# Optimization experiments

Hardware: AMD Instinct MI355X
Metric: run time of the kernel (lower is better)

## Reference

```python
import jax, jax.numpy as jnp
import numpy as np

B, M, D, H, C = 256, 512, 768, 8, 768


def setup_inputs() -> dict:
    key = jax.random.key(0)
    ks = jax.random.split(key, 12)
    rn = lambda k, shp, s=1.0: jax.random.normal(k, shp, dtype=jnp.float32) * s
    w = 1.0 / np.sqrt(D)
    return dict(
        controller_state=rn(ks[0], (B, C)),
        write_data=rn(ks[1], (B, D)),
        memory=rn(ks[2], (M, D), 0.1),
        in_proj_w=rn(ks[3], (3 * D, D), w), in_proj_b=jnp.zeros((3 * D,), jnp.float32),
        out_w=rn(ks[4], (D, D), w), out_b=jnp.zeros((D,), jnp.float32),
        read_w=rn(ks[5], (D, C), w), read_b=jnp.zeros((D,), jnp.float32),
        write_w=rn(ks[6], (D, C), w), write_b=jnp.zeros((D,), jnp.float32),
        erase_w=rn(ks[7], (D, C), w), erase_b=jnp.zeros((D,), jnp.float32),
        ug_w=rn(ks[8], (1, C + D), w), ug_b=jnp.zeros((1,), jnp.float32),
        fg_w=rn(ks[9], (1, C + D), w), fg_b=jnp.zeros((1,), jnp.float32),
    )


def _mha(q, kv, in_proj_w, in_proj_b, out_w, out_b, num_heads):
    # q: [B,1,D] query, kv: [B,M,D] keys=values. Matches torch.nn.MultiheadAttention
    # (batch_first, eval mode -> no dropout, average_attn_weights=True).
    b, m, d = kv.shape
    dh = d // num_heads
    wq, wk, wv = jnp.split(in_proj_w, 3, axis=0)
    bq, bk, bv = jnp.split(in_proj_b, 3, axis=0)
    qh = (q @ wq.T + bq).reshape(b, 1, num_heads, dh).transpose(0, 2, 1, 3)   # [B,H,1,dh]
    kh = (kv @ wk.T + bk).reshape(b, m, num_heads, dh).transpose(0, 2, 1, 3)  # [B,H,M,dh]
    vh = (kv @ wv.T + bv).reshape(b, m, num_heads, dh).transpose(0, 2, 1, 3)
    scores = jnp.einsum('bhqd,bhkd->bhqk', qh, kh) / jnp.sqrt(jnp.float32(dh))
    attn = jax.nn.softmax(scores, axis=-1)                                    # [B,H,1,M]
    ctx = jnp.einsum('bhqk,bhkd->bhqd', attn, vh)
    ctx = ctx.transpose(0, 2, 1, 3).reshape(b, 1, d)
    out = ctx @ out_w.T + out_b
    return out, attn.mean(axis=1)  # out [B,1,D], weights averaged over heads [B,1,M]


def reference(controller_state, write_data, memory, in_proj_w, in_proj_b,
              out_w, out_b, read_w, read_b, write_w, write_b,
              erase_w, erase_b, ug_w, ug_b, fg_w, fg_b):
    b = controller_state.shape[0]
    memory_batch = jnp.broadcast_to(memory[None], (b,) + memory.shape)        # [B,M,D]

    read_key = (controller_state @ read_w.T + read_b)[:, None, :]             # [B,1,D]
    read_data, _ = _mha(read_key, memory_batch, in_proj_w, in_proj_b, out_w, out_b, H)
    read_data = read_data[:, 0, :]                                            # [B,D]

    write_key = (controller_state @ write_w.T + write_b)[:, None, :]
    erase_vec = jax.nn.sigmoid(controller_state @ erase_w.T + erase_b)[:, None, :]  # [B,1,D]
    _, write_weights = _mha(write_key, memory_batch, in_proj_w, in_proj_b, out_w, out_b, H)
    ww = write_weights[:, 0, :]                                               # [B,M]

    combined = jnp.concatenate([controller_state, read_data], axis=-1)        # [B,C+D]
    ug = jax.nn.sigmoid(combined @ ug_w.T + ug_b)                             # [B,1]
    fg = jax.nn.sigmoid(combined @ fg_w.T + fg_b)                             # [B,1]

    erase_term = ww[:, :, None] * erase_vec * fg[:, :, None]                  # [B,M,D]
    write_term = ww[:, :, None] * write_data[:, None, :] * ug[:, :, None]     # [B,M,D]
    updated_memory = memory_batch + (write_term - erase_term)
    return read_data, updated_memory
```

## Files before the change

### kernel.cpp

```cpp
#include <hip/hip_runtime.h>
#include <math.h>

#define B_ 256
#define M_ 512
#define D_ 768
#define H_ 8
#define DH_ 96
#define C_ 768

typedef float  f32x4_t __attribute__((ext_vector_type(4)));
typedef short  s16x8   __attribute__((ext_vector_type(8)));
typedef unsigned short u16;

__device__ __forceinline__ u16 cvt_bf16(float f) {
    union { float f; unsigned int u; } v; v.f = f;
    unsigned int r = (v.u + 0x7FFFu + ((v.u >> 16) & 1u)) >> 16;
    return (u16)r;
}
__device__ __forceinline__ float bf16_f32(u16 h) {
    union { unsigned int u; float f; } v; v.u = ((unsigned int)h) << 16;
    return v.f;
}

#define ACC_INIT {{0,0,0,0},{0,0,0,0},{0,0,0,0},{0,0,0,0}}

__global__ __launch_bounds__(256) void conv_bf16(
    const float* __restrict__ mem, const float* __restrict__ cs,
    const float* __restrict__ ipw, const float* __restrict__ rw,
    const float* __restrict__ www, const float* __restrict__ ew,
    const float* __restrict__ outw,
    u16* __restrict__ memb, u16* __restrict__ csb, u16* __restrict__ ipwb,
    u16* __restrict__ rwb, u16* __restrict__ wwwb, u16* __restrict__ ewb,
    u16* __restrict__ outwb)
{
    const int bid = blockIdx.x;
    const float* src; u16* dst; int base;
    if      (bid < 192)  { src = mem;  dst = memb;  base = bid; }
    else if (bid < 288)  { src = cs;   dst = csb;   base = bid - 192; }
    else if (bid < 1152) { src = ipw;  dst = ipwb;  base = bid - 288; }
    else if (bid < 1440) { src = rw;   dst = rwb;   base = bid - 1152; }
    else if (bid < 1728) { src = www;  dst = wwwb;  base = bid - 1440; }
    else if (bid < 2016) { src = ew;   dst = ewb;   base = bid - 1728; }
    else                 { src = outw; dst = outwb; base = bid - 2016; }
    const size_t i = ((size_t)base * 256 + threadIdx.x) * 8;
    float4 x = *reinterpret_cast<const float4*>(src + i);
    float4 y = *reinterpret_cast<const float4*>(src + i + 4);
    s16x8 o;
    o[0]=cvt_bf16(x.x); o[1]=cvt_bf16(x.y); o[2]=cvt_bf16(x.z); o[3]=cvt_bf16(x.w);
    o[4]=cvt_bf16(y.x); o[5]=cvt_bf16(y.y); o[6]=cvt_bf16(y.z); o[7]=cvt_bf16(y.w);
    *reinterpret_cast<s16x8*>(dst + i) = o;
}

template<int BK>
__device__ __forceinline__ void mm64b(
    const u16* __restrict__ A, int lda, const u16* __restrict__ B, int ldb,
    int ksteps, int bRowClamp, u16* lA, u16* lB, f32x4_t* acc, int nfrag)
{
    constexpr int NL = BK / 32;
    const int t = threadIdx.x;
    const int srow = t >> 2, kq = t & 3;
    const int l = t & 63, w = t >> 6;
    const int brow = srow < bRowClamp ? srow : bRowClamp;

    for (int ks = 0; ks < ksteps; ++ks) {
        s16x8 va[NL], vb[NL];
        #pragma unroll
        for (int c = 0; c < NL; ++c) {
            const int ko = ks * BK + (kq * NL + c) * 8;
            va[c] = *reinterpret_cast<const s16x8*>(A + (size_t)srow * lda + ko);
            vb[c] = *reinterpret_cast<const s16x8*>(B + (size_t)brow * ldb + ko);
        }
        __syncthreads();
        #pragma unroll
        for (int c = 0; c < NL; ++c) {
            const int kb = kq * NL + c;
            *reinterpret_cast<s16x8*>(lA + (kb * 64 + srow) * 8) = va[c];
            *reinterpret_cast<s16x8*>(lB + (kb * 64 + srow) * 8) = vb[c];
        }
        __syncthreads();
        #pragma unroll
        for (int ksub = 0; ksub < NL; ++ksub) {
            const int kb = (l >> 4) + ksub * 4;
            s16x8 af = *reinterpret_cast<const s16x8*>(lA + (kb * 64 + w * 16 + (l & 15)) * 8);
            #pragma unroll
            for (int nb = 0; nb < 4; ++nb) {
                if (nb < nfrag) {
                    s16x8 bf = *reinterpret_cast<const s16x8*>(lB + (kb * 64 + nb * 16 + (l & 15)) * 8);
                    acc[nb] = __builtin_amdgcn_mfma_f32_16x16x32_bf16(af, bf, acc[nb], 0, 0, 0);
                }
            }
        }
    }
}

__device__ __forceinline__ void epilogue_f32(
    const f32x4_t* acc, float* out, int ldo, int m0, int n0,
    const float* bias, int act, int nfrag)
{
    const int t = threadIdx.x, l = t & 63, w = t >> 6;
    const int mbase = m0 + w * 16 + (l >> 4) * 4;
    #pragma unroll
    for (int nb = 0; nb < 4; ++nb) {
        if (nb >= nfrag) break;
        const int col = n0 + nb * 16 + (l & 15);
        const float bv = bias ? bias[col] : 0.0f;
        #pragma unroll
        for (int r = 0; r < 4; ++r) {
            float v = acc[nb][r] + bv;
            if (act) v = 1.0f / (1.0f + expf(-v));
            out[(size_t)(mbase + r) * ldo + col] = v;
        }
    }
}

__device__ __forceinline__ void epilogue_bf16(
    const f32x4_t* acc, u16* out, int ldo, int m0, int n0,
    const float* bias, float scale, int nfrag)
{
    const int t = threadIdx.x, l = t & 63, w = t >> 6;
    const int mbase = m0 + w * 16 + (l >> 4) * 4;
    #pragma unroll
    for (int nb = 0; nb < 4; ++nb) {
        if (nb >= nfrag) break;
        const int col = n0 + nb * 16 + (l & 15);
        const float bv = bias ? bias[col] : 0.0f;
        #pragma unroll
        for (int r = 0; r < 4; ++r)
            out[(size_t)(mbase + r) * ldo + col] = cvt_bf16(acc[nb][r] * scale + bv);
    }
}

__global__ __launch_bounds__(256) void stage1_mfma(
    const u16* __restrict__ memb, const u16* __restrict__ csb,
    const u16* __restrict__ ipwb, const float* __restrict__ ipb,
    const u16* __restrict__ rwb, const float* __restrict__ rb,
    const u16* __restrict__ wwwb, const float* __restrict__ ww_b,
    const u16* __restrict__ ewb, const float* __restrict__ eb,
    u16* __restrict__ khb, u16* __restrict__ vhT,
    u16* __restrict__ rwkeysb, float* __restrict__ erase)
{
    __shared__ u16 lA[8192], lB[8192];
    f32x4_t acc[4] = ACC_INIT;
    const int bid = blockIdx.x;
    if (bid < 192) {
        const int mt = bid / 24, nt = bid % 24;
        mm64b<64>(memb + (size_t)mt * 64 * 768, 768,
                  ipwb + (size_t)768 * 768 + (size_t)nt * 64 * 768, 768,
                  12, 63, lA, lB, acc, 4);
        const int t = threadIdx.x, l = t & 63, w = t >> 6;
        const int mbase = mt * 64 + w * 16 + (l >> 4) * 4;
        if (nt < 12) {
            #pragma unroll
            for (int nb = 0; nb < 4; ++nb) {
                const int col = nt * 64 + nb * 16 + (l & 15);
                const float bv = ipb[768 + col];
                #pragma unroll
                for (int r = 0; r < 4; ++r)
                    khb[(size_t)(mbase + r) * 768 + col] = cvt_bf16(acc[nb][r] + bv);
            }
        } else {
            #pragma unroll
            for (int nb = 0; nb < 4; ++nb) {
                const int cg = (nt - 12) * 64 + nb * 16 + (l & 15);
                const int h = cg / 96, d = cg % 96;
                const float bv = ipb[1536 + cg];
                u16* dst = vhT + ((size_t)h * 96 + d) * 512;
                #pragma unroll
                for (int r = 0; r < 4; ++r)
                    dst[mbase + r] = cvt_bf16(acc[nb][r] + bv);
            }
        }
    } else if (bid < 240) {
        const int lid = bid - 192, mt = lid / 12, nt = lid % 12;
        mm64b<64>(csb + (size_t)mt * 64 * 768, 768, rwb + (size_t)nt * 64 * 768, 768,
                  12, 63, lA, lB, acc, 4);
        epilogue_bf16(acc, rwkeysb, 768, mt * 64, nt * 64, rb, 1.0f, 4);
    } else if (bid < 288) {
        const int lid = bid - 240, mt = lid / 12, nt = lid % 12;
        mm64b<64>(csb + (size_t)mt * 64 * 768, 768, wwwb + (size_t)nt * 64 * 768, 768,
                  12, 63, lA, lB, acc, 4);
        epilogue_bf16(acc, rwkeysb + (size_t)256 * 768, 768, mt * 64, nt * 64, ww_b, 1.0f, 4);
    } else {
        const int lid = bid - 288, mt = lid / 12, nt = lid % 12;
        mm64b<64>(csb + (size_t)mt * 64 * 768, 768, ewb + (size_t)nt * 64 * 768, 768,
                  12, 63, lA, lB, acc, 4);
        epilogue_f32(acc, erase, 768, mt * 64, nt * 64, eb, 1, 4);
    }
}

__global__ __launch_bounds__(256) void stage2_mfma(
    const u16* __restrict__ rwkeysb, const u16* __restrict__ ipwb,
    const float* __restrict__ ipb, u16* __restrict__ qrwb)
{
    __shared__ u16 lA[8192], lB[8192];
    f32x4_t acc[4] = ACC_INIT;
    const int mt = blockIdx.x / 12, nt = blockIdx.x % 12;
    mm64b<64>(rwkeysb + (size_t)mt * 64 * 768, 768, ipwb + (size_t)nt * 64 * 768, 768,
              12, 63, lA, lB, acc, 4);
    epilogue_bf16(acc, qrwb, 768, mt * 64, nt * 64, ipb, 1.0f, 4);
}

__global__ __launch_bounds__(256) void scores_mfma(
    const u16* __restrict__ qrwb, const u16* __restrict__ khb, u16* __restrict__ S)
{
    __shared__ u16 lA[4096], lB[4096];
    f32x4_t acc[4] = ACC_INIT;
    const int h = blockIdx.y;
    const int mt = blockIdx.x >> 3, nt = blockIdx.x & 7;
    mm64b<32>(qrwb + (size_t)mt * 64 * 768 + h * 96, 768,
              khb + (size_t)nt * 64 * 768 + h * 96, 768, 3, 63, lA, lB, acc, 4);
    epilogue_bf16(acc, S + (size_t)h * 512 * 512, 512, mt * 64, nt * 64,
                  nullptr, 0.10206207261596577f, 4);
}

__global__ __launch_bounds__(256) void softmax_rows(
    const u16* __restrict__ S, u16* __restrict__ Pr, float* __restrict__ attnw)
{
    const int rid = blockIdx.x, h = rid >> 9, q = rid & 511, t = threadIdx.x;
    __shared__ float red4[4];
    const u16* s = S + (size_t)rid * 512;
    const float s0 = bf16_f32(s[t]), s1 = bf16_f32(s[t + 256]);
    float v = fmaxf(s0, s1);
    #pragma unroll
    for (int off = 32; off > 0; off >>= 1) v = fmaxf(v, __shfl_xor(v, off));
    if ((t & 63) == 0) red4[t >> 6] = v;
    __syncthreads();
    const float mx = fmaxf(fmaxf(red4[0], red4[1]), fmaxf(red4[2], red4[3]));
    float e0 = expf(s0 - mx), e1 = expf(s1 - mx);
    float sum = e0 + e1;
    #pragma unroll
    for (int off = 32; off > 0; off >>= 1) sum += __shfl_xor(sum, off);
    __syncthreads();
    if ((t & 63) == 0) red4[t >> 6] = sum;
    __syncthreads();
    const float inv = 1.0f / (red4[0] + red4[1] + red4[2] + red4[3]);
    e0 *= inv; e1 *= inv;
    if (q < 256) {
        u16* p = Pr + ((size_t)(h * 256 + q)) * 512;
        p[t] = cvt_bf16(e0); p[t + 256] = cvt_bf16(e1);
    } else {
        float* a = attnw + ((size_t)(q - 256) * 8 + h) * 512;
        a[t] = e0; a[t + 256] = e1;
    }
}

__global__ __launch_bounds__(256) void pv_mfma(
    const u16* __restrict__ Pr, const u16* __restrict__ vhT, u16* __restrict__ ctxb)
{
    __shared__ u16 lA[8192], lB[8192];
    f32x4_t acc[4] = ACC_INIT;
    const int h = blockIdx.z, mt = blockIdx.x, nt = blockIdx.y;
    const int n0 = nt * 64;
    const int nfrag = nt == 0 ? 4 : 2;
    const int bclamp = nt == 0 ? 63 : 31;
    mm64b<64>(Pr + ((size_t)h * 256 + mt * 64) * 512, 512,
              vhT + ((size_t)h * 96 + n0) * 512, 512, 8, bclamp, lA, lB, acc, nfrag);
    epilogue_bf16(acc, ctxb + h * 96, 768, mt * 64, n0, nullptr, 1.0f, nfrag);
}

__global__ __launch_bounds__(256) void stage4_mfma(
    const u16* __restrict__ ctxb, const u16* __restrict__ outwb,
    const float* __restrict__ outb, float* __restrict__ rd_out,
    const float* __restrict__ attnw, float* __restrict__ ww)
{
    __shared__ u16 lA[8192], lB[8192];
    const int bid = blockIdx.x;
    if (bid < 48) {
        f32x4_t acc[4] = ACC_INIT;
        const int mt = bid / 12, nt = bid % 12;
        mm64b<64>(ctxb + (size_t)mt * 64 * 768, 768, outwb + (size_t)nt * 64 * 768, 768,
                  12, 63, lA, lB, acc, 4);
        epilogue_f32(acc, rd_out, 768, mt * 64, nt * 64, outb, 0, 4);
    } else {
        const int i = (bid - 48) * 256 + threadIdx.x;
        const int b = i >> 9, m = i & 511;
        float s = 0.f;
        #pragma unroll
        for (int h = 0; h < H_; ++h)
            s += attnw[((size_t)b * H_ + h) * M_ + m];
        ww[i] = s * 0.125f;
    }
}

__global__ __launch_bounds__(256) void gates_delta(
    const float* __restrict__ cs, const float* __restrict__ rd,
    const float* __restrict__ wdta, const float* __restrict__ ev,
    const float* __restrict__ ugw, const float* __restrict__ ugb,
    const float* __restrict__ fgw, const float* __restrict__ fgb,
    float* __restrict__ delta)
{
    const int b = blockIdx.x, t = threadIdx.x;
    __shared__ float red4[4];
    __shared__ float gates[2];

    float pu = 0.f, pf = 0.f;
    for (int i = t; i < C_; i += 256) {
        const float c = cs[(size_t)b * C_ + i];
        pu += c * ugw[i];
        pf += c * fgw[i];
    }
    for (int i = t; i < D_; i += 256) {
        const float r = rd[(size_t)b * D_ + i];
        pu += r * ugw[C_ + i];
        pf += r * fgw[C_ + i];
    }
    #pragma unroll
    for (int off = 32; off > 0; off >>= 1) pu += __shfl_xor(pu, off);
    if ((t & 63) == 0) red4[t >> 6] = pu;
    __syncthreads();
    if (t == 0) gates[0] = 1.0f / (1.0f + expf(-(red4[0] + red4[1] + red4[2] + red4[3] + ugb[0])));
    __syncthreads();
    #pragma unroll
    for (int off = 32; off > 0; off >>= 1) pf += __shfl_xor(pf, off);
    if ((t & 63) == 0) red4[t >> 6] = pf;
    __syncthreads();
    if (t == 0) gates[1] = 1.0f / (1.0f + expf(-(red4[0] + red4[1] + red4[2] + red4[3] + fgb[0])));
    __syncthreads();

    const float ug = gates[0], fg = gates[1];
    for (int d = t; d < D_; d += 256)
        delta[(size_t)b * D_ + d] = wdta[(size_t)b * D_ + d] * ug - ev[(size_t)b * D_ + d] * fg;
}

__global__ __launch_bounds__(192) void update_mem(
    const float* __restrict__ mem, const float* __restrict__ ww,
    const float* __restrict__ delta, float* __restrict__ out)
{
    const int blk = blockIdx.x;
    const int b   = blk >> 6;
    const int m0  = (blk & 63) << 3;
    const int t   = threadIdx.x;

    const f32x4_t d4 = *reinterpret_cast<const f32x4_t*>(delta + (size_t)b * D_ + t * 4);
    const f32x4_t* m4 = reinterpret_cast<const f32x4_t*>(mem);
    f32x4_t* o4 = reinterpret_cast<f32x4_t*>(out + (size_t)b * M_ * D_);

    #pragma unroll
    for (int i = 0; i < 8; ++i) {
        const int m = m0 + i;
        const float w = ww[(size_t)b * M_ + m];
        f32x4_t mm = m4[(size_t)m * 192 + t];
        f32x4_t r = mm + w * d4;
        __builtin_nontemporal_store(r, &o4[(size_t)m * 192 + t]);
    }
}

extern "C" void kernel_launch(void* const* d_in, const int* in_sizes, int n_in,
                              void* d_out, int out_size, void* d_ws, size_t ws_size,
                              hipStream_t stream)
{
    const float* cs   = (const float*)d_in[0];
    const float* wdta = (const float*)d_in[1];
    const float* mem  = (const float*)d_in[2];
    const float* ipw  = (const float*)d_in[3];
    const float* ipb  = (const float*)d_in[4];
    const float* outw = (const float*)d_in[5];
    const float* outb = (const float*)d_in[6];
    const float* rw   = (const float*)d_in[7];
    const float* rb   = (const float*)d_in[8];
    const float* ww_w = (const float*)d_in[9];
    const float* ww_b = (const float*)d_in[10];
    const float* ew   = (const float*)d_in[11];
    const float* eb   = (const float*)d_in[12];
    const float* ugw  = (const float*)d_in[13];
    const float* ugb  = (const float*)d_in[14];
    const float* fgw  = (const float*)d_in[15];
    const float* fgb  = (const float*)d_in[16];

    float* rd_out  = (float*)d_out;
    float* mem_out = (float*)d_out + B_ * D_;

    float* S0 = mem_out;
    u16*   khb     = (u16*)(S0 + 0);
    u16*   vhT     = (u16*)(S0 + 196608);
    u16*   rwkeysb = (u16*)(S0 + 393216);
    u16*   qrwb    = (u16*)(S0 + 589824);
    u16*   Sb      = (u16*)(S0 + 786432);
    u16*   Prb     = (u16*)(S0 + 1835008);
    float* attnw   =        S0 + 2359296;
    u16*   ctxb    = (u16*)(S0 + 3407872);
    float* erase   =        S0 + 3506176;
    u16*   memb    = (u16*)(S0 + 3702784);
    u16*   csb     = (u16*)(S0 + 3899392);
    u16*   ipwb    = (u16*)(S0 + 3997696);
    u16*   rwb     = (u16*)(S0 + 4882432);
    u16*   wwwb    = (u16*)(S0 + 5177344);
    u16*   ewb     = (u16*)(S0 + 5472256);
    u16*   outwb   = (u16*)(S0 + 5767168);

    float* wwb   = (float*)d_ws;
    float* delta = wwb + B_ * M_;

    conv_bf16<<<2304, 256, 0, stream>>>(mem, cs, ipw, rw, ww_w, ew, outw,
                                        memb, csb, ipwb, rwb, wwwb, ewb, outwb);
    stage1_mfma<<<336, 256, 0, stream>>>(memb, csb, ipwb, ipb, rwb, rb, wwwb, ww_b,
                                         ewb, eb, khb, vhT, rwkeysb, erase);
    stage2_mfma<<<96, 256, 0, stream>>>(rwkeysb, ipwb, ipb, qrwb);
    scores_mfma<<<dim3(64, 8), 256, 0, stream>>>(qrwb, khb, Sb);
    softmax_rows<<<4096, 256, 0, stream>>>(Sb, Prb, attnw);
    pv_mfma<<<dim3(4, 2, 8), 256, 0, stream>>>(Prb, vhT, ctxb);
    stage4_mfma<<<560, 256, 0, stream>>>(ctxb, outwb, outb, rd_out, attnw, wwb);
    gates_delta<<<B_, 256, 0, stream>>>(cs, rd_out, wdta, erase, ugw, ugb, fgw, fgb, delta);
    update_mem<<<B_ * (M_ / 8), 192, 0, stream>>>(mem, wwb, delta, mem_out);
}
```

Measured before the change: 146.5 us.

## Fold query projections into weights, fuse scores with softmax, and fold gates through out_proj

Precomputes the combined weights Wq·read_w and Wq·write_w, plus their biases, in a prep kernel. This removes the dependent second projection GEMM stage. Scores and softmax are fused into one kernel that writes unnormalized exponentials without a max subtraction (the exponent is clamped at 30) together with per-row inverse sums, so the separate score and probability buffers go away. The gate logits are computed from ctx through a precomputed out_w·gate vector, so the gate kernel no longer waits on read_data, and it is merged with the output projection and the head-averaging kernel. Dropping the max subtraction risks accuracy for large scores, and the weight-folding GEMMs are recomputed on every call.

```diff
diff --git a/kernel.cpp b/kernel.cpp
--- a/kernel.cpp
+++ b/kernel.cpp
@@ -10,6 +10,7 @@
 
 typedef float  f32x4_t __attribute__((ext_vector_type(4)));
 typedef short  s16x8   __attribute__((ext_vector_type(8)));
+typedef short  s16x4   __attribute__((ext_vector_type(4)));
 typedef unsigned short u16;
 
 __device__ __forceinline__ u16 cvt_bf16(float f) {
@@ -23,33 +24,7 @@
 }
 
 #define ACC_INIT {{0,0,0,0},{0,0,0,0},{0,0,0,0},{0,0,0,0}}
-
-__global__ __launch_bounds__(256) void conv_bf16(
-    const float* __restrict__ mem, const float* __restrict__ cs,
-    const float* __restrict__ ipw, const float* __restrict__ rw,
-    const float* __restrict__ www, const float* __restrict__ ew,
-    const float* __restrict__ outw,
-    u16* __restrict__ memb, u16* __restrict__ csb, u16* __restrict__ ipwb,
-    u16* __restrict__ rwb, u16* __restrict__ wwwb, u16* __restrict__ ewb,
-    u16* __restrict__ outwb)
-{
-    const int bid = blockIdx.x;
-    const float* src; u16* dst; int base;
-    if      (bid < 192)  { src = mem;  dst = memb;  base = bid; }
-    else if (bid < 288)  { src = cs;   dst = csb;   base = bid - 192; }
-    else if (bid < 1152) { src = ipw;  dst = ipwb;  base = bid - 288; }
-    else if (bid < 1440) { src = rw;   dst = rwb;   base = bid - 1152; }
-    else if (bid < 1728) { src = www;  dst = wwwb;  base = bid - 1440; }
-    else if (bid < 2016) { src = ew;   dst = ewb;   base = bid - 1728; }
-    else                 { src = outw; dst = outwb; base = bid - 2016; }
-    const size_t i = ((size_t)base * 256 + threadIdx.x) * 8;
-    float4 x = *reinterpret_cast<const float4*>(src + i);
-    float4 y = *reinterpret_cast<const float4*>(src + i + 4);
-    s16x8 o;
-    o[0]=cvt_bf16(x.x); o[1]=cvt_bf16(x.y); o[2]=cvt_bf16(x.z); o[3]=cvt_bf16(x.w);
-    o[4]=cvt_bf16(y.x); o[5]=cvt_bf16(y.y); o[6]=cvt_bf16(y.z); o[7]=cvt_bf16(y.w);
-    *reinterpret_cast<s16x8*>(dst + i) = o;
-}
+#define SCALE_ 0.10206207261596577f
 
 template<int BK>
 __device__ __forceinline__ void mm64b(
@@ -115,7 +90,7 @@
 
 __device__ __forceinline__ void epilogue_bf16(
     const f32x4_t* acc, u16* out, int ldo, int m0, int n0,
-    const float* bias, float scale, int nfrag)
+    const float* bias, int nfrag)
 {
     const int t = threadIdx.x, l = t & 63, w = t >> 6;
     const int mbase = m0 + w * 16 + (l >> 4) * 4;
@@ -126,18 +101,136 @@
         const float bv = bias ? bias[col] : 0.0f;
         #pragma unroll
         for (int r = 0; r < 4; ++r)
-            out[(size_t)(mbase + r) * ldo + col] = cvt_bf16(acc[nb][r] * scale + bv);
-    }
-}
-
-__global__ __launch_bounds__(256) void stage1_mfma(
+            out[(size_t)(mbase + r) * ldo + col] = cvt_bf16(acc[nb][r] + bv);
+    }
+}
+
+__device__ __forceinline__ void mmT64(
+    const float* __restrict__ A, const float* __restrict__ Bt,
+    int m0, int n0, u16* lA, u16* lB, f32x4_t* acc)
+{
+    const int t = threadIdx.x;
+    const int arow = t >> 2, akq = t & 3;
+    const int bkrow = t >> 3, bnq = t & 7;
+    const int l = t & 63, w = t >> 6;
+
+    for (int ks = 0; ks < 24; ++ks) {
+        const float* pa = A + (size_t)(m0 + arow) * 768 + ks * 32 + akq * 8;
+        float4 xa = *reinterpret_cast<const float4*>(pa);
+        float4 ya = *reinterpret_cast<const float4*>(pa + 4);
+        const float* pb = Bt + (size_t)(ks * 32 + bkrow) * 768 + n0 + bnq * 8;
+        float4 xb = *reinterpret_cast<const float4*>(pb);
+        float4 yb = *reinterpret_cast<const float4*>(pb + 4);
+        __syncthreads();
+        s16x8 va;
+        va[0]=cvt_bf16(xa.x); va[1]=cvt_bf16(xa.y); va[2]=cvt_bf16(xa.z); va[3]=cvt_bf16(xa.w);
+        va[4]=cvt_bf16(ya.x); va[5]=cvt_bf16(ya.y); va[6]=cvt_bf16(ya.z); va[7]=cvt_bf16(ya.w);
+        *reinterpret_cast<s16x8*>(lA + (akq * 64 + arow) * 8) = va;
+        u16 vb[8];
+        vb[0]=cvt_bf16(xb.x); vb[1]=cvt_bf16(xb.y); vb[2]=cvt_bf16(xb.z); vb[3]=cvt_bf16(xb.w);
+        vb[4]=cvt_bf16(yb.x); vb[5]=cvt_bf16(yb.y); vb[6]=cvt_bf16(yb.z); vb[7]=cvt_bf16(yb.w);
+        const int kb = bkrow >> 3, j = bkrow & 7;
+        #pragma unroll
+        for (int i = 0; i < 8; ++i)
+            lB[(kb * 64 + bnq * 8 + i) * 8 + j] = vb[i];
+        __syncthreads();
+        const int kk = l >> 4;
+        s16x8 af = *reinterpret_cast<const s16x8*>(lA + (kk * 64 + w * 16 + (l & 15)) * 8);
+        #pragma unroll
+        for (int nb = 0; nb < 4; ++nb) {
+            s16x8 bf = *reinterpret_cast<const s16x8*>(lB + (kk * 64 + nb * 16 + (l & 15)) * 8);
+            acc[nb] = __builtin_amdgcn_mfma_f32_16x16x32_bf16(af, bf, acc[nb], 0, 0, 0);
+        }
+    }
+}
+
+__global__ __launch_bounds__(256) void prep_kernel(
+    const float* __restrict__ mem, const float* __restrict__ cs,
+    const float* __restrict__ ipw, const float* __restrict__ ipb,
+    const float* __restrict__ rw, const float* __restrict__ rb,
+    const float* __restrict__ www, const float* __restrict__ ww_b,
+    const float* __restrict__ ew, const float* __restrict__ outw,
+    const float* __restrict__ outb,
+    const float* __restrict__ ugw, const float* __restrict__ ugb,
+    const float* __restrict__ fgw, const float* __restrict__ fgb,
+    u16* __restrict__ memb, u16* __restrict__ csb, u16* __restrict__ ipwb,
+    u16* __restrict__ ewb, u16* __restrict__ outwb,
+    u16* __restrict__ Wqr, u16* __restrict__ Wqw,
+    float* __restrict__ bqr, float* __restrict__ bqw,
+    float* __restrict__ vg, float* __restrict__ gc)
+{
+    __shared__ u16 lA[2048], lB[2048];
+    __shared__ float sred[256];
+    const int bid = blockIdx.x, t = threadIdx.x;
+
+    if (bid < 1440) {
+        const float* src; u16* dst; int base;
+        if      (bid < 192)  { src = mem;            dst = memb;  base = bid; }
+        else if (bid < 288)  { src = cs;             dst = csb;   base = bid - 192; }
+        else if (bid < 864)  { src = ipw + 589824;   dst = ipwb;  base = bid - 288; }
+        else if (bid < 1152) { src = ew;             dst = ewb;   base = bid - 864; }
+        else                 { src = outw;           dst = outwb; base = bid - 1152; }
+        const size_t i = ((size_t)base * 256 + t) * 8;
+        float4 x = *reinterpret_cast<const float4*>(src + i);
+        float4 y = *reinterpret_cast<const float4*>(src + i + 4);
+        s16x8 o;
+        o[0]=cvt_bf16(x.x); o[1]=cvt_bf16(x.y); o[2]=cvt_bf16(x.z); o[3]=cvt_bf16(x.w);
+        o[4]=cvt_bf16(y.x); o[5]=cvt_bf16(y.y); o[6]=cvt_bf16(y.z); o[7]=cvt_bf16(y.w);
+        *reinterpret_cast<s16x8*>(dst + i) = o;
+    } else if (bid < 1728) {
+        const int lid = bid - 1440;
+        const int tgt = lid / 144, r = lid % 144;
+        const int mt = r / 12, nt = r % 12;
+        f32x4_t acc[4] = ACC_INIT;
+        mmT64(ipw, tgt == 0 ? rw : www, mt * 64, nt * 64, lA, lB, acc);
+        epilogue_bf16(acc, tgt == 0 ? Wqr : Wqw, 768, mt * 64, nt * 64, nullptr, 4);
+    } else if (bid < 2112) {
+        const int lid = bid - 1728;
+        const int vec = lid / 192, rr = lid % 192;
+        const int w = t >> 6, l = t & 63;
+        const int j = rr * 4 + w;
+        const float* dv = vec == 0 ? rb : ww_b;
+        const float* wqr_ = ipw + (size_t)j * 768 + l * 12;
+        float s = 0.f;
+        #pragma unroll
+        for (int c = 0; c < 3; ++c) {
+            float4 a = *reinterpret_cast<const float4*>(wqr_ + c * 4);
+            float4 b = *reinterpret_cast<const float4*>(dv + l * 12 + c * 4);
+            s += a.x * b.x + a.y * b.y + a.z * b.z + a.w * b.w;
+        }
+        #pragma unroll
+        for (int off = 32; off > 0; off >>= 1) s += __shfl_xor(s, off);
+        if (l == 0) (vec == 0 ? bqr : bqw)[j] = s + ipb[j];
+    } else {
+        const int v = bid - 2112;
+        const float* gw = v == 0 ? ugw : fgw;
+        float a0 = 0.f, a1 = 0.f, a2 = 0.f;
+        for (int j = 0; j < 768; ++j) {
+            const float s = gw[768 + j];
+            const float* row = outw + (size_t)j * 768;
+            a0 += row[t] * s; a1 += row[t + 256] * s; a2 += row[t + 512] * s;
+        }
+        vg[v * 768 + t] = a0; vg[v * 768 + t + 256] = a1; vg[v * 768 + t + 512] = a2;
+        float cpart = outb[t] * gw[768 + t] + outb[t + 256] * gw[768 + t + 256]
+                    + outb[t + 512] * gw[768 + t + 512];
+        sred[t] = cpart; __syncthreads();
+        #pragma unroll
+        for (int off = 128; off > 0; off >>= 1) {
+            if (t < off) sred[t] += sred[t + off];
+            __syncthreads();
+        }
+        if (t == 0) gc[v] = sred[0] + (v == 0 ? ugb[0] : fgb[0]);
+    }
+}
+
+__global__ __launch_bounds__(256) void proj_kernel(
     const u16* __restrict__ memb, const u16* __restrict__ csb,
     const u16* __restrict__ ipwb, const float* __restrict__ ipb,
-    const u16* __restrict__ rwb, const float* __restrict__ rb,
-    const u16* __restrict__ wwwb, const float* __restrict__ ww_b,
+    const u16* __restrict__ Wqr, const float* __restrict__ bqr,
+    const u16* __restrict__ Wqw, const float* __restrict__ bqw,
     const u16* __restrict__ ewb, const float* __restrict__ eb,
     u16* __restrict__ khb, u16* __restrict__ vhT,
-    u16* __restrict__ rwkeysb, float* __restrict__ erase)
+    u16* __restrict__ qrwb, float* __restrict__ erase)
 {
     __shared__ u16 lA[8192], lB[8192];
     f32x4_t acc[4] = ACC_INIT;
@@ -145,8 +238,7 @@
     if (bid < 192) {
         const int mt = bid / 24, nt = bid % 24;
         mm64b<64>(memb + (size_t)mt * 64 * 768, 768,
-                  ipwb + (size_t)768 * 768 + (size_t)nt * 64 * 768, 768,
-                  12, 63, lA, lB, acc, 4);
+                  ipwb + (size_t)nt * 64 * 768, 768, 12, 63, lA, lB, acc, 4);
         const int t = threadIdx.x, l = t & 63, w = t >> 6;
         const int mbase = mt * 64 + w * 16 + (l >> 4) * 4;
         if (nt < 12) {
@@ -172,14 +264,14 @@
         }
     } else if (bid < 240) {
         const int lid = bid - 192, mt = lid / 12, nt = lid % 12;
-        mm64b<64>(csb + (size_t)mt * 64 * 768, 768, rwb + (size_t)nt * 64 * 768, 768,
+        mm64b<64>(csb + (size_t)mt * 64 * 768, 768, Wqr + (size_t)nt * 64 * 768, 768,
                   12, 63, lA, lB, acc, 4);
-        epilogue_bf16(acc, rwkeysb, 768, mt * 64, nt * 64, rb, 1.0f, 4);
+        epilogue_bf16(acc, qrwb, 768, mt * 64, nt * 64, bqr, 4);
     } else if (bid < 288) {
         const int lid = bid - 240, mt = lid / 12, nt = lid % 12;
-        mm64b<64>(csb + (size_t)mt * 64 * 768, 768, wwwb + (size_t)nt * 64 * 768, 768,
+        mm64b<64>(csb + (size_t)mt * 64 * 768, 768, Wqw + (size_t)nt * 64 * 768, 768,
                   12, 63, lA, lB, acc, 4);
-        epilogue_bf16(acc, rwkeysb + (size_t)256 * 768, 768, mt * 64, nt * 64, ww_b, 1.0f, 4);
+        epilogue_bf16(acc, qrwb + (size_t)256 * 768, 768, mt * 64, nt * 64, bqw, 4);
     } else {
         const int lid = bid - 288, mt = lid / 12, nt = lid % 12;
         mm64b<64>(csb + (size_t)mt * 64 * 768, 768, ewb + (size_t)nt * 64 * 768, 768,
@@ -188,64 +280,77 @@
     }
 }
 
-__global__ __launch_bounds__(256) void stage2_mfma(
-    const u16* __restrict__ rwkeysb, const u16* __restrict__ ipwb,
-    const float* __restrict__ ipb, u16* __restrict__ qrwb)
-{
-    __shared__ u16 lA[8192], lB[8192];
-    f32x4_t acc[4] = ACC_INIT;
-    const int mt = blockIdx.x / 12, nt = blockIdx.x % 12;
-    mm64b<64>(rwkeysb + (size_t)mt * 64 * 768, 768, ipwb + (size_t)nt * 64 * 768, 768,
-              12, 63, lA, lB, acc, 4);
-    epilogue_bf16(acc, qrwb, 768, mt * 64, nt * 64, ipb, 1.0f, 4);
-}
-
-__global__ __launch_bounds__(256) void scores_mfma(
-    const u16* __restrict__ qrwb, const u16* __restrict__ khb, u16* __restrict__ S)
-{
-    __shared__ u16 lA[4096], lB[4096];
-    f32x4_t acc[4] = ACC_INIT;
-    const int h = blockIdx.y;
-    const int mt = blockIdx.x >> 3, nt = blockIdx.x & 7;
-    mm64b<32>(qrwb + (size_t)mt * 64 * 768 + h * 96, 768,
-              khb + (size_t)nt * 64 * 768 + h * 96, 768, 3, 63, lA, lB, acc, 4);
-    epilogue_bf16(acc, S + (size_t)h * 512 * 512, 512, mt * 64, nt * 64,
-                  nullptr, 0.10206207261596577f, 4);
-}
-
-__global__ __launch_bounds__(256) void softmax_rows(
-    const u16* __restrict__ S, u16* __restrict__ Pr, float* __restrict__ attnw)
-{
-    const int rid = blockIdx.x, h = rid >> 9, q = rid & 511, t = threadIdx.x;
-    __shared__ float red4[4];
-    const u16* s = S + (size_t)rid * 512;
-    const float s0 = bf16_f32(s[t]), s1 = bf16_f32(s[t + 256]);
-    float v = fmaxf(s0, s1);
+__global__ __launch_bounds__(256) void scores_sm_kernel(
+    const u16* __restrict__ qrwb, const u16* __restrict__ khb,
+    u16* __restrict__ E, float* __restrict__ linv)
+{
+    __shared__ u16 Kl[512 * 104];
+    __shared__ u16 Ql[64 * 104];
+    __shared__ float lred[256];
+
+    const int qt = blockIdx.x, h = blockIdx.y, t = threadIdx.x;
+    const int l = t & 63, w = t >> 6;
+
+    for (int c = t; c < 512 * 12; c += 256) {
+        const int m = c / 12, dc = c % 12;
+        s16x8 v = *reinterpret_cast<const s16x8*>(khb + (size_t)m * 768 + h * 96 + dc * 8);
+        *reinterpret_cast<s16x8*>(Kl + m * 104 + dc * 8) = v;
+    }
+    for (int c = t; c < 64 * 12; c += 256) {
+        const int q = c / 12, dc = c % 12;
+        s16x8 v = *reinterpret_cast<const s16x8*>(qrwb + (size_t)(qt * 64 + q) * 768 + h * 96 + dc * 8);
+        *reinterpret_cast<s16x8*>(Ql + q * 104 + dc * 8) = v;
+    }
+    __syncthreads();
+
+    float l_acc[4] = {0.f, 0.f, 0.f, 0.f};
+
+    for (int mt = 0; mt < 8; ++mt) {
+        f32x4_t acc[4] = ACC_INIT;
+        #pragma unroll
+        for (int ks = 0; ks < 3; ++ks) {
+            s16x8 af = *reinterpret_cast<const s16x8*>(
+                Kl + (mt * 64 + w * 16 + (l & 15)) * 104 + ks * 32 + (l >> 4) * 8);
+            #pragma unroll
+            for (int nb = 0; nb < 4; ++nb) {
+                s16x8 bf = *reinterpret_cast<const s16x8*>(
+                    Ql + (nb * 16 + (l & 15)) * 104 + ks * 32 + (l >> 4) * 8);
+                acc[nb] = __builtin_amdgcn_mfma_f32_16x16x32_bf16(af, bf, acc[nb], 0, 0, 0);
+            }
+        }
+        const int mbase = mt * 64 + w * 16 + (l >> 4) * 4;
+        #pragma unroll
+        for (int nb = 0; nb < 4; ++nb) {
+            const int q = qt * 64 + nb * 16 + (l & 15);
+            s16x4 pk;
+            float e0 = expf(fminf(acc[nb][0] * SCALE_, 30.0f));
+            float e1 = expf(fminf(acc[nb][1] * SCALE_, 30.0f));
+            float e2 = expf(fminf(acc[nb][2] * SCALE_, 30.0f));
+            float e3 = expf(fminf(acc[nb][3] * SCALE_, 30.0f));
+            l_acc[nb] += (e0 + e1) + (e2 + e3);
+            pk[0] = cvt_bf16(e0); pk[1] = cvt_bf16(e1);
+            pk[2] = cvt_bf16(e2); pk[3] = cvt_bf16(e3);
+            *reinterpret_cast<s16x4*>(E + ((size_t)h * 512 + q) * 512 + mbase) = pk;
+        }
+    }
+
     #pragma unroll
-    for (int off = 32; off > 0; off >>= 1) v = fmaxf(v, __shfl_xor(v, off));
-    if ((t & 63) == 0) red4[t >> 6] = v;
+    for (int nb = 0; nb < 4; ++nb) {
+        float v = l_acc[nb];
+        v += __shfl_xor(v, 16);
+        v += __shfl_xor(v, 32);
+        if (l < 16) lred[w * 64 + nb * 16 + l] = v;
+    }
     __syncthreads();
-    const float mx = fmaxf(fmaxf(red4[0], red4[1]), fmaxf(red4[2], red4[3]));
-    float e0 = expf(s0 - mx), e1 = expf(s1 - mx);
-    float sum = e0 + e1;
-    #pragma unroll
-    for (int off = 32; off > 0; off >>= 1) sum += __shfl_xor(sum, off);
-    __syncthreads();
-    if ((t & 63) == 0) red4[t >> 6] = sum;
-    __syncthreads();
-    const float inv = 1.0f / (red4[0] + red4[1] + red4[2] + red4[3]);
-    e0 *= inv; e1 *= inv;
-    if (q < 256) {
-        u16* p = Pr + ((size_t)(h * 256 + q)) * 512;
-        p[t] = cvt_bf16(e0); p[t + 256] = cvt_bf16(e1);
-    } else {
-        float* a = attnw + ((size_t)(q - 256) * 8 + h) * 512;
-        a[t] = e0; a[t + 256] = e1;
-    }
-}
-
-__global__ __launch_bounds__(256) void pv_mfma(
-    const u16* __restrict__ Pr, const u16* __restrict__ vhT, u16* __restrict__ ctxb)
+    if (t < 64) {
+        const float s = lred[t] + lred[64 + t] + lred[128 + t] + lred[192 + t];
+        linv[h * 512 + qt * 64 + t] = 1.0f / s;
+    }
+}
+
+__global__ __launch_bounds__(256) void pv_kernel(
+    const u16* __restrict__ E, const float* __restrict__ linv,
+    const u16* __restrict__ vhT, u16* __restrict__ ctxb)
 {
     __shared__ u16 lA[8192], lB[8192];
     f32x4_t acc[4] = ACC_INIT;
@@ -253,73 +358,77 @@
     const int n0 = nt * 64;
     const int nfrag = nt == 0 ? 4 : 2;
     const int bclamp = nt == 0 ? 63 : 31;
-    mm64b<64>(Pr + ((size_t)h * 256 + mt * 64) * 512, 512,
+    mm64b<64>(E + ((size_t)h * 512 + mt * 64) * 512, 512,
               vhT + ((size_t)h * 96 + n0) * 512, 512, 8, bclamp, lA, lB, acc, nfrag);
-    epilogue_bf16(acc, ctxb + h * 96, 768, mt * 64, n0, nullptr, 1.0f, nfrag);
-}
-
-__global__ __launch_bounds__(256) void stage4_mfma(
+    const int t = threadIdx.x, l = t & 63, w = t >> 6;
+    const int mbase = mt * 64 + w * 16 + (l >> 4) * 4;
+    #pragma unroll
+    for (int nb = 0; nb < 4; ++nb) {
+        if (nb >= nfrag) break;
+        const int col = n0 + nb * 16 + (l & 15);
+        #pragma unroll
+        for (int r = 0; r < 4; ++r) {
+            const float lv = linv[h * 512 + mbase + r];
+            ctxb[(size_t)(mbase + r) * 768 + h * 96 + col] = cvt_bf16(acc[nb][r] * lv);
+        }
+    }
+}
+
+__global__ __launch_bounds__(256) void finalize_kernel(
     const u16* __restrict__ ctxb, const u16* __restrict__ outwb,
     const float* __restrict__ outb, float* __restrict__ rd_out,
-    const float* __restrict__ attnw, float* __restrict__ ww)
+    const float* __restrict__ cs, const float* __restrict__ wdta,
+    const float* __restrict__ erase,
+    const float* __restrict__ ugw, const float* __restrict__ fgw,
+    const float* __restrict__ vg, const float* __restrict__ gc,
+    const u16* __restrict__ E, const float* __restrict__ linv,
+    float* __restrict__ delta, float* __restrict__ wwb)
 {
     __shared__ u16 lA[8192], lB[8192];
-    const int bid = blockIdx.x;
+    const int bid = blockIdx.x, t = threadIdx.x;
     if (bid < 48) {
         f32x4_t acc[4] = ACC_INIT;
         const int mt = bid / 12, nt = bid % 12;
         mm64b<64>(ctxb + (size_t)mt * 64 * 768, 768, outwb + (size_t)nt * 64 * 768, 768,
                   12, 63, lA, lB, acc, 4);
         epilogue_f32(acc, rd_out, 768, mt * 64, nt * 64, outb, 0, 4);
+    } else if (bid < 304) {
+        const int b = bid - 48;
+        __shared__ float red[8];
+        float pu = 0.f, pf = 0.f;
+        #pragma unroll
+        for (int c = 0; c < 3; ++c) {
+            const int i = t + c * 256;
+            const float cv = cs[(size_t)b * 768 + i];
+            const float xv = bf16_f32(ctxb[(size_t)b * 768 + i]);
+            pu += cv * ugw[i] + xv * vg[i];
+            pf += cv * fgw[i] + xv * vg[768 + i];
+        }
+        const int w = t >> 6, l = t & 63;
+        #pragma unroll
+        for (int off = 32; off > 0; off >>= 1) {
+            pu += __shfl_xor(pu, off);
+            pf += __shfl_xor(pf, off);
+        }
+        if (l == 0) { red[w] = pu; red[4 + w] = pf; }
+        __syncthreads();
+        const float ug = 1.0f / (1.0f + expf(-(red[0] + red[1] + red[2] + red[3] + gc[0])));
+        const float fg = 1.0f / (1.0f + expf(-(red[4] + red[5] + red[6] + red[7] + gc[1])));
+        #pragma unroll
+        for (int c = 0; c < 3; ++c) {
+            const int i = t + c * 256;
+            delta[(size_t)b * 768 + i] = wdta[(size_t)b * 768 + i] * ug
+                                       - erase[(size_t)b * 768 + i] * fg;
+        }
     } else {
-        const int i = (bid - 48) * 256 + threadIdx.x;
-        const int b = i >> 9, m = i & 511;
+        const int idx = (bid - 304) * 256 + t;
+        const int b = idx >> 9, m = idx & 511;
         float s = 0.f;
         #pragma unroll
         for (int h = 0; h < H_; ++h)
-            s += attnw[((size_t)b * H_ + h) * M_ + m];
-        ww[i] = s * 0.125f;
-    }
-}
-
-__global__ __launch_bounds__(256) void gates_delta(
-    const float* __restrict__ cs, const float* __restrict__ rd,
-    const float* __restrict__ wdta, const float* __restrict__ ev,
-    const float* __restrict__ ugw, const float* __restrict__ ugb,
-    const float* __restrict__ fgw, const float* __restrict__ fgb,
-    float* __restrict__ delta)
-{
-    const int b = blockIdx.x, t = threadIdx.x;
-    __shared__ float red4[4];
-    __shared__ float gates[2];
-
-    float pu = 0.f, pf = 0.f;
-    for (int i = t; i < C_; i += 256) {
-        const float c = cs[(size_t)b * C_ + i];
-        pu += c * ugw[i];
-        pf += c * fgw[i];
-    }
-    for (int i = t; i < D_; i += 256) {
-        const float r = rd[(size_t)b * D_ + i];
-        pu += r * ugw[C_ + i];
-        pf += r * fgw[C_ + i];
-    }
-    #pragma unroll
-    for (int off = 32; off > 0; off >>= 1) pu += __shfl_xor(pu, off);
-    if ((t & 63) == 0) red4[t >> 6] = pu;
-    __syncthreads();
-    if (t == 0) gates[0] = 1.0f / (1.0f + expf(-(red4[0] + red4[1] + red4[2] + red4[3] + ugb[0])));
-    __syncthreads();
-    #pragma unroll
-    for (int off = 32; off > 0; off >>= 1) pf += __shfl_xor(pf, off);
-    if ((t & 63) == 0) red4[t >> 6] = pf;
-    __syncthreads();
-    if (t == 0) gates[1] = 1.0f / (1.0f + expf(-(red4[0] + red4[1] + red4[2] + red4[3] + fgb[0])));
-    __syncthreads();
-
-    const float ug = gates[0], fg = gates[1];
-    for (int d = t; d < D_; d += 256)
-        delta[(size_t)b * D_ + d] = wdta[(size_t)b * D_ + d] * ug - ev[(size_t)b * D_ + d] * fg;
+            s += bf16_f32(E[((size_t)h * 512 + 256 + b) * 512 + m]) * linv[h * 512 + 256 + b];
+        wwb[(size_t)b * 512 + m] = s * 0.125f;
+    }
 }
 
 __global__ __launch_bounds__(192) void update_mem(
@@ -371,35 +480,39 @@
     float* mem_out = (float*)d_out + B_ * D_;
 
     float* S0 = mem_out;
-    u16*   khb     = (u16*)(S0 + 0);
-    u16*   vhT     = (u16*)(S0 + 196608);
-    u16*   rwkeysb = (u16*)(S0 + 393216);
-    u16*   qrwb    = (u16*)(S0 + 589824);
-    u16*   Sb      = (u16*)(S0 + 786432);
-    u16*   Prb     = (u16*)(S0 + 1835008);
-    float* attnw   =        S0 + 2359296;
-    u16*   ctxb    = (u16*)(S0 + 3407872);
-    float* erase   =        S0 + 3506176;
-    u16*   memb    = (u16*)(S0 + 3702784);
-    u16*   csb     = (u16*)(S0 + 3899392);
-    u16*   ipwb    = (u16*)(S0 + 3997696);
-    u16*   rwb     = (u16*)(S0 + 4882432);
-    u16*   wwwb    = (u16*)(S0 + 5177344);
-    u16*   ewb     = (u16*)(S0 + 5472256);
-    u16*   outwb   = (u16*)(S0 + 5767168);
-
-    float* wwb   = (float*)d_ws;
-    float* delta = wwb + B_ * M_;
-
-    conv_bf16<<<2304, 256, 0, stream>>>(mem, cs, ipw, rw, ww_w, ew, outw,
-                                        memb, csb, ipwb, rwb, wwwb, ewb, outwb);
-    stage1_mfma<<<336, 256, 0, stream>>>(memb, csb, ipwb, ipb, rwb, rb, wwwb, ww_b,
-                                         ewb, eb, khb, vhT, rwkeysb, erase);
-    stage2_mfma<<<96, 256, 0, stream>>>(rwkeysb, ipwb, ipb, qrwb);
-    scores_mfma<<<dim3(64, 8), 256, 0, stream>>>(qrwb, khb, Sb);
-    softmax_rows<<<4096, 256, 0, stream>>>(Sb, Prb, attnw);
-    pv_mfma<<<dim3(4, 2, 8), 256, 0, stream>>>(Prb, vhT, ctxb);
-    stage4_mfma<<<560, 256, 0, stream>>>(ctxb, outwb, outb, rd_out, attnw, wwb);
-    gates_delta<<<B_, 256, 0, stream>>>(cs, rd_out, wdta, erase, ugw, ugb, fgw, fgb, delta);
+    u16*   memb  = (u16*)(S0 + 0);
+    u16*   csb   = (u16*)(S0 + 196608);
+    u16*   ipwb  = (u16*)(S0 + 294912);
+    u16*   ewb   = (u16*)(S0 + 884736);
+    u16*   outwb = (u16*)(S0 + 1179648);
+    u16*   Wqr   = (u16*)(S0 + 1474560);
+    u16*   Wqw   = (u16*)(S0 + 1769472);
+    float* bqr   =        S0 + 2064384;
+    float* bqw   =        S0 + 2065152;
+    u16*   khb   = (u16*)(S0 + 2065920);
+    u16*   vhT   = (u16*)(S0 + 2262528);
+    u16*   qrwb  = (u16*)(S0 + 2459136);
+
+    float* ws    = (float*)d_ws;
+    float* erase = ws;
+    u16*   ctxb  = (u16*)(ws + 196608);
+    u16*   E     = (u16*)(ws + 294912);
+    float* linv  =        ws + 1343488;
+    float* vg    =        ws + 1347584;
+    float* gc    =        ws + 1349120;
+    float* delta =        ws + 1349136;
+    float* wwb   =        ws + 1545744;
+
+    prep_kernel<<<2114, 256, 0, stream>>>(mem, cs, ipw, ipb, rw, rb, ww_w, ww_b,
+                                          ew, outw, outb, ugw, ugb, fgw, fgb,
+                                          memb, csb, ipwb, ewb, outwb,
+                                          Wqr, Wqw, bqr, bqw, vg, gc);
+    proj_kernel<<<336, 256, 0, stream>>>(memb, csb, ipwb, ipb, Wqr, bqr, Wqw, bqw,
+                                         ewb, eb, khb, vhT, qrwb, erase);
+    scores_sm_kernel<<<dim3(8, 8), 256, 0, stream>>>(qrwb, khb, E, linv);
+    pv_kernel<<<dim3(4, 2, 8), 256, 0, stream>>>(E, linv, vhT, ctxb);
+    finalize_kernel<<<816, 256, 0, stream>>>(ctxb, outwb, outb, rd_out,
+                                             cs, wdta, erase, ugw, fgw, vg, gc,
+                                             E, linv, delta, wwb);
     update_mem<<<B_ * (M_ / 8), 192, 0, stream>>>(mem, wwb, delta, mem_out);
 }
```

After: 173.5 us. 1.18x slower.
